# Kernel tuning notes

Measured on AMD Instinct MI355X. Metric: run time of the kernel, lower is better.

## Reference

```python
import jax, jax.numpy as jnp
import numpy as np

B, T, D_IN, D_OUT, D_CTX, A_HID, L_CTX = 32, 256, 512, 512, 512, 512, 128


def setup_inputs() -> dict:
    key = jax.random.key(0)
    ks = jax.random.split(key, 10)
    s = 0.05  # small init scale to avoid gate saturation
    return {
        "x": jax.random.normal(ks[0], (B, T, D_IN), jnp.float32),
        "context": jax.random.normal(ks[1], (B, L_CTX, D_CTX), jnp.float32),
        "W": jax.random.normal(ks[2], (D_IN, 4 * D_OUT), jnp.float32) * s,
        "V": jax.random.normal(ks[3], (D_CTX, 4 * D_OUT), jnp.float32) * s,
        "U": jax.random.normal(ks[4], (D_OUT, 4 * D_OUT), jnp.float32) * s,
        "b": jnp.concatenate([
            jnp.zeros((D_OUT,), jnp.float32),        # b_i
            jnp.ones((D_OUT,), jnp.float32),         # b_f (forget bias init = ones)
            jnp.zeros((2 * D_OUT,), jnp.float32),    # b_c, b_o
        ]),
        "W_h_att": jax.random.normal(ks[5], (D_OUT, A_HID), jnp.float32) * s,
        "W_ctx_att": jax.random.normal(ks[6], (D_CTX, A_HID), jnp.float32) * s,
        "b_att": jnp.zeros((A_HID,), jnp.float32),
        "w_att_prj": jax.random.normal(ks[7], (A_HID, 1), jnp.float32) * s,
    }


def reference(x, context, W, V, U, b, W_h_att, W_ctx_att, b_att, w_att_prj):
    D = U.shape[0]  # output_dim
    # Precompute attention-projected context: (B, L, A)
    att_ctx = jnp.einsum("blc,ca->bla", context, W_ctx_att) + b_att
    # Precompute input contribution for all timesteps: (B, T, 4D)
    xW = jnp.einsum("btd,dk->btk", x, W)

    h0 = jnp.zeros((x.shape[0], D), x.dtype)
    c0 = jnp.zeros((x.shape[0], D), x.dtype)

    def step(carry, xw_t):
        h, c = carry
        # soft attention over context
        h_att = h @ W_h_att                                  # (B, A)
        preprj = jnp.tanh(h_att[:, None, :] + att_ctx)        # (B, L, A)
        prj = jnp.squeeze(preprj @ w_att_prj, -1)             # (B, L)
        alpha = jax.nn.softmax(prj, axis=-1)
        wctx = jnp.einsum("bl,blc->bc", alpha, context)       # (B, C)
        # LSTM gates; slice order follows the original step():
        # i=0, f=1, o=slice 2, candidate=slice 3
        preact = xw_t + wctx @ V + h @ U + b                  # (B, 4D)
        i = jax.nn.sigmoid(preact[:, :D])
        f = jax.nn.sigmoid(preact[:, D:2 * D])
        o = jax.nn.sigmoid(preact[:, 2 * D:3 * D])
        cand = jnp.tanh(preact[:, 3 * D:])
        c_new = f * c + i * cand
        h_new = o * jnp.tanh(c_new)
        return (h_new, c_new), h_new

    xw_seq = jnp.swapaxes(xW, 0, 1)                           # (T, B, 4D)
    _, hs = jax.lax.scan(step, (h0, c0), xw_seq)
    return jnp.swapaxes(hs, 0, 1)                             # (B, T, D)
```

## Files before the change

### kernel.cpp

```cpp
#include <hip/hip_runtime.h>
#include <hip/hip_fp16.h>

#define GD 256
#define BD 1024

constexpr int TSTEPS = 256;
constexpr int DD = 512;
constexpr int LC = 128;

constexpr size_t OFF_FLAGS_F = 0;
constexpr size_t OFF_REL_F   = 8192;
constexpr size_t OFF_GFLG_F  = 8448;
constexpr size_t OFF_HUX     = 16640;
constexpr size_t OFF_SCP     = 82176;
constexpr size_t OFF_H16_F   = 213248;
constexpr size_t HO_HX    = 0;
constexpr size_t HO_ATT   = 16384;
constexpr size_t HO_U16   = 2113536;
constexpr size_t HO_WH16  = 3162112;
constexpr size_t HO_CTXV  = 3424256;
constexpr size_t HO_XW    = 11812864;

typedef _Float16 h16;
typedef _Float16 h2  __attribute__((ext_vector_type(2)));
typedef _Float16 h8v __attribute__((ext_vector_type(8)));
union H8  { h8v v; h2 p[4]; };
union H2U { h2 h; unsigned u; };
union HSU { h16 h; unsigned short u; };

__device__ __forceinline__ float rcp_fast(float x) { return __builtin_amdgcn_rcpf(x); }
__device__ __forceinline__ float ftanh(float x) {
  float e = __expf(2.0f * x);
  return 1.0f - 2.0f * rcp_fast(e + 1.0f);
}
__device__ __forceinline__ float fsig(float x) { return rcp_fast(1.0f + __expf(-x)); }
__device__ __forceinline__ float fdot2(h2 a, h2 b, float c) {
  return __builtin_amdgcn_fdot2(a, b, c, false);
}

__device__ __forceinline__ float cloadf(const float* p) {
  return __hip_atomic_load(p, __ATOMIC_RELAXED, __HIP_MEMORY_SCOPE_AGENT);
}
__device__ __forceinline__ unsigned cloadu(const unsigned* p) {
  return __hip_atomic_load(p, __ATOMIC_RELAXED, __HIP_MEMORY_SCOPE_AGENT);
}
__device__ __forceinline__ void cstoref(float* p, float v) {
  __hip_atomic_store(p, v, __ATOMIC_RELAXED, __HIP_MEMORY_SCOPE_AGENT);
}
__device__ __forceinline__ void cstoreu(unsigned* p, unsigned v) {
  __hip_atomic_store(p, v, __ATOMIC_RELAXED, __HIP_MEMORY_SCOPE_AGENT);
}
__device__ __forceinline__ void cstoreu8(unsigned long long* p, unsigned long long v) {
  __hip_atomic_store(p, v, __ATOMIC_RELAXED, __HIP_MEMORY_SCOPE_AGENT);
}
__device__ __forceinline__ void cstores(h16* p, h16 v) {
  HSU s; s.h = v;
  __hip_atomic_store((unsigned short*)p, s.u, __ATOMIC_RELAXED,
                     __HIP_MEMORY_SCOPE_AGENT);
}

__device__ __forceinline__ void gsync(int* flags, int* rel, int w, int& gen) {
  __syncthreads();
  gen++;
  const int t = threadIdx.x;
  if (w == 0) {
    if (t < 64) {
      if (t == 0)
        __hip_atomic_store(flags, gen, __ATOMIC_RELAXED, __HIP_MEMORY_SCOPE_AGENT);
      for (;;) {
        int m = gen;
#pragma unroll
        for (int i = 0; i < 4; i++) {
          int v = __hip_atomic_load(flags + (t + i * 64) * 32,
                                    __ATOMIC_RELAXED, __HIP_MEMORY_SCOPE_AGENT);
          m = (v < m) ? v : m;
        }
        if (__all(m >= gen)) break;
      }
      if (t == 0) {
#pragma unroll
        for (int i = 0; i < 8; i++)
          __hip_atomic_store(rel + i * 32, gen, __ATOMIC_RELAXED,
                             __HIP_MEMORY_SCOPE_AGENT);
      }
    }
    asm volatile("" ::: "memory");
  } else {
    if (t == 0) {
      __hip_atomic_store(flags + w * 32, gen, __ATOMIC_RELAXED,
                         __HIP_MEMORY_SCOPE_AGENT);
      const int* r = rel + (w & 7) * 32;
      while (__hip_atomic_load(r, __ATOMIC_RELAXED, __HIP_MEMORY_SCOPE_AGENT) < gen)
        __builtin_amdgcn_s_sleep(1);
    }
    asm volatile("" ::: "memory");
  }
  __syncthreads();
}

__device__ __forceinline__ void gbar32(int* gf, int j, int& sg) {
  __syncthreads();
  sg++;
  const int t = threadIdx.x;
  if (t < 64) {
    if (t == 0)
      __hip_atomic_store(gf + j * 32, sg, __ATOMIC_RELAXED,
                         __HIP_MEMORY_SCOPE_AGENT);
    for (;;) {
      int v = sg;
      if (t < 32)
        v = __hip_atomic_load(gf + t * 32, __ATOMIC_RELAXED,
                              __HIP_MEMORY_SCOPE_AGENT);
      if (__all(v >= sg)) break;
      __builtin_amdgcn_s_sleep(1);
    }
  }
  asm volatile("" ::: "memory");
  __syncthreads();
}

__global__ __launch_bounds__(BD, 4) void attn_lstm_persistent(
    const float* __restrict__ x, const float* __restrict__ ctx,
    const float* __restrict__ W, const float* __restrict__ V,
    const float* __restrict__ U, const float* __restrict__ bias,
    const float* __restrict__ Wh, const float* __restrict__ Wc,
    const float* __restrict__ batt, const float* __restrict__ wprj,
    float* __restrict__ out, float* __restrict__ ws) {
  __shared__ __align__(16) unsigned char smem[58448];
  h16*   attcL = (h16*)smem;
  float* red   = (float*)(smem + 18432);
  float* red2  = (float*)(smem + 34816);
  h2*    hLDS  = (h2*)(smem + 51200);
  float* sl    = (float*)(smem + 55296);
  h2*    anL   = (h2*)(smem + 55808);
  float* hattL = (float*)(smem + 56064);
  float* wpL   = (float*)(smem + 56320);
  float* biasS = (float*)(smem + 56384);
  float* pre   = (float*)(smem + 57408);
  float* zinvS = (float*)(smem + 58432);

  const int w = blockIdx.x;
  const int t = threadIdx.x;
  const int xg = w & 7;
  const int j  = w >> 3;
  const int q2 = j >> 3;
  const int bb = 4 * xg + q2;
  const int oct = j & 7;

  int* flags = (int*)(ws + OFF_FLAGS_F);
  int* rel   = (int*)(ws + OFF_REL_F);
  int* gfl   = (int*)(ws + OFF_GFLG_F) + xg * 1024;
  float* hUX = ws + OFF_HUX;
  float* scP = ws + OFF_SCP;
  h16* hb16  = (h16*)(ws + OFF_H16_F);
  h16* hX    = hb16 + HO_HX;
  h16* att16 = hb16 + HO_ATT;
  h16* ctxVp = hb16 + HO_CTXV;
  h16* xw16  = hb16 + HO_XW;

  int gen = 0, sg = 0;
  float c_reg = 0.f;

  {
    const int kp = w;
    {
      const float* r0p = U + (size_t)(2 * kp) * 2048;
      const float* r1p = r0p + 2048;
      const int col0 = 2 * t;
      float u00 = r0p[col0], u01 = r0p[col0 + 1];
      float u10 = r1p[col0], u11 = r1p[col0 + 1];
      int oc  = (col0 & 511) >> 6;
      int cc0 = ((col0 >> 9) << 6) | (col0 & 63);
      H2U p0; p0.h = h2{(h16)u00, (h16)u10};
      H2U p1; p1.h = h2{(h16)u01, (h16)u11};
      unsigned long long pk =
          (unsigned long long)p0.u | ((unsigned long long)p1.u << 32);
      cstoreu8((unsigned long long*)((h2*)(hb16 + HO_U16) +
                                     (size_t)oc * 65536 + (size_t)kp * 256 + cc0),
               pk);
    }
    if (t < 512) {
      float w0 = Wh[(size_t)(2 * kp) * DD + t];
      float w1 = Wh[(size_t)(2 * kp + 1) * DD + t];
      H2U pu; pu.h = h2{(h16)w0, (h16)w1};
      cstoreu((unsigned*)((h2*)(hb16 + HO_WH16) + (size_t)(t >> 6) * 16384 +
                          (size_t)kp * 64 + (t & 63)),
              pu.u);
    }
  }
  {
    float* fbuf = (float*)smem;
    const int r0 = w * 16;
#pragma unroll
    for (int i = 0; i < 2; i++) {
      int idx4 = i * BD + t;
      int row = idx4 >> 7, c4 = idx4 & 127;
      ((float4*)fbuf)[idx4] = ((const float4*)(ctx + (size_t)(r0 + row) * DD))[c4];
    }
    __syncthreads();
    const int a0 = t & 511, rh = t >> 9;
    float acc[8];
#pragma unroll
    for (int r = 0; r < 8; r++) acc[r] = 0.f;
    for (int cc = 0; cc < DD; cc++) {
      float wv = Wc[(size_t)cc * DD + a0];
#pragma unroll
      for (int r = 0; r < 8; r++)
        acc[r] += fbuf[(8 * rh + r) * DD + cc] * wv;
    }
    const float ba = batt[a0];
    for (int r = 0; r < 8; r++)
      cstores(att16 + (size_t)(r0 + 8 * rh + r) * DD + a0, (h16)(acc[r] + ba));
    __syncthreads();
  }
  {
    const int bS = w >> 3, octS = w & 7;
    h2* xstage = (h2*)smem;
    for (int chk = 0; chk < 8; chk++) {
      const int st0 = chk * 32;
      {
        const int row = t >> 5, seg = t & 31;
        const float* src = x + ((size_t)bS * TSTEPS + st0 + row) * DD + seg * 16;
        h2* dst = xstage + row * 256 + seg * 8;
#pragma unroll
        for (int q = 0; q < 4; q++) {
          float4 v = *(const float4*)(src + 4 * q);
          dst[2 * q]     = h2{(h16)v.x, (h16)v.y};
          dst[2 * q + 1] = h2{(h16)v.z, (h16)v.w};
        }
      }
      __syncthreads();
      const int cc = t & 255, sq = t >> 8;
      const int col = ((cc >> 6) << 9) + 64 * octS + (cc & 63);
      float acc[8];
#pragma unroll
      for (int jj = 0; jj < 8; jj++) acc[jj] = 0.f;
#pragma unroll 2
      for (int kp = 0; kp < 256; kp++) {
        float w0 = W[(size_t)(2 * kp) * 2048 + col];
        float w1 = W[(size_t)(2 * kp + 1) * 2048 + col];
        h2 wp = h2{(h16)w0, (h16)w1};
#pragma unroll
        for (int jj = 0; jj < 8; jj++)
          acc[jj] = fdot2(xstage[(sq * 8 + jj) * 256 + kp], wp, acc[jj]);
      }
#pragma unroll
      for (int jj = 0; jj < 8; jj++)
        cstores(xw16 + (((size_t)(bS * 8 + octS) * 256) + st0 + sq * 8 + jj) * 256 + cc,
                (h16)acc[jj]);
      __syncthreads();
    }
    for (int chk = 0; chk < 4; chk++) {
      const int l0 = chk * 32;
      {
        const int row = t >> 5, seg = t & 31;
        const float* src = ctx + ((size_t)bS * LC + l0 + row) * DD + seg * 16;
        h2* dst = xstage + row * 256 + seg * 8;
#pragma unroll
        for (int q = 0; q < 4; q++) {
          float4 v = *(const float4*)(src + 4 * q);
          dst[2 * q]     = h2{(h16)v.x, (h16)v.y};
          dst[2 * q + 1] = h2{(h16)v.z, (h16)v.w};
        }
      }
      __syncthreads();
      const int cc = t & 255, lq = t >> 8;
      const int col = ((cc >> 6) << 9) + 64 * octS + (cc & 63);
      float acc[8];
#pragma unroll
      for (int jj = 0; jj < 8; jj++) acc[jj] = 0.f;
#pragma unroll 2
      for (int kp = 0; kp < 256; kp++) {
        float v0 = V[(size_t)(2 * kp) * 2048 + col];
        float v1 = V[(size_t)(2 * kp + 1) * 2048 + col];
        h2 vp = h2{(h16)v0, (h16)v1};
#pragma unroll
        for (int jj = 0; jj < 8; jj++)
          acc[jj] = fdot2(xstage[(lq * 8 + jj) * 256 + kp], vp, acc[jj]);
      }
#pragma unroll
      for (int jj = 0; jj < 8; jj++)
        cstores(ctxVp + (((size_t)(bS * 8 + octS) * 128) + l0 + lq * 8 + jj) * 256 + cc,
                (h16)acc[jj]);
      __syncthreads();
    }
  }
  gsync(flags, rel, w, gen);

  const int ccL = t & 63, kseg = t >> 6;
  const int aL = t & 15, ks2 = t >> 4;
  h2 u[16], wh[4], cvp01[8], cvp23[8];
  {
    const h2* Ub = (const h2*)(hb16 + HO_U16) + (size_t)(j & 7) * 65536 +
                   (size_t)(j >> 3) * 64 + ccL;
#pragma unroll
    for (int i = 0; i < 16; i++) u[i] = Ub[(size_t)(16 * kseg + i) * 256];
    const h2* Wb = (const h2*)(hb16 + HO_WH16) + (size_t)(j >> 2) * 16384 +
                   16 * (j & 3) + aL;
#pragma unroll
    for (int i = 0; i < 4; i++) wh[i] = Wb[(size_t)(4 * ks2 + i) * 64];
  }
  {
    const int ccg = t & 31, lq = t >> 5;
    const h16* cvb = ctxVp + ((size_t)(bb * 8 + oct) * 128) * 256 + ccg * 8;
    H8 p0, p1, p2, p3;
    p0.v = *(const h8v*)(cvb + (size_t)(4 * lq + 0) * 256);
    p1.v = *(const h8v*)(cvb + (size_t)(4 * lq + 1) * 256);
    p2.v = *(const h8v*)(cvb + (size_t)(4 * lq + 2) * 256);
    p3.v = *(const h8v*)(cvb + (size_t)(4 * lq + 3) * 256);
#pragma unroll
    for (int j8 = 0; j8 < 8; j8++) {
      cvp01[j8] = h2{p0.v[j8], p1.v[j8]};
      cvp23[j8] = h2{p2.v[j8], p3.v[j8]};
    }
  }
  {
    const int row = t >> 1, half = t & 1, q = row >> 7, l = row & 127;
    uint4 v = *(const uint4*)(att16 + (size_t)((4 * xg + q) * LC + l) * DD +
                              16 * j + 8 * half);
    unsigned* dp = (unsigned*)(attcL + row * 18 + 8 * half);
    dp[0] = v.x; dp[1] = v.y; dp[2] = v.z; dp[3] = v.w;
  }
  if (t < 16) wpL[t] = wprj[16 * j + t];
  if (t < 256) biasS[t] = bias[(size_t)(t >> 6) * 512 + 64 * oct + (t & 63)];
  __syncthreads();

  for (int step = 0; step < TSTEPS; step++) {
    {
      unsigned hv = 0;
      if (step > 0)
        hv = cloadu((const unsigned*)(hX + (size_t)(4 * xg + (t >> 8)) * DD +
                                      2 * (t & 255)));
      ((unsigned*)hLDS)[t] = hv;
      __syncthreads();
      {
        float f0 = 0.f, f1 = 0.f, f2 = 0.f, f3 = 0.f;
        const int base = 16 * kseg;
#pragma unroll
        for (int i = 0; i < 16; i++) {
          h2 uu = u[i];
          f0 = fdot2(hLDS[base + i], uu, f0);
          f1 = fdot2(hLDS[256 + base + i], uu, f1);
          f2 = fdot2(hLDS[512 + base + i], uu, f2);
          f3 = fdot2(hLDS[768 + base + i], uu, f3);
        }
        red[kseg * 256 + ccL]       = f0;
        red[kseg * 256 + 64 + ccL]  = f1;
        red[kseg * 256 + 128 + ccL] = f2;
        red[kseg * 256 + 192 + ccL] = f3;
      }
      {
        float g0 = 0.f, g1 = 0.f, g2 = 0.f, g3 = 0.f;
        const int base = 4 * ks2;
#pragma unroll
        for (int i = 0; i < 4; i++) {
          h2 ww = wh[i];
          g0 = fdot2(hLDS[base + i], ww, g0);
          g1 = fdot2(hLDS[256 + base + i], ww, g1);
          g2 = fdot2(hLDS[512 + base + i], ww, g2);
          g3 = fdot2(hLDS[768 + base + i], ww, g3);
        }
        red2[ks2 * 64 + aL]      = g0;
        red2[ks2 * 64 + 16 + aL] = g1;
        red2[ks2 * 64 + 32 + aL] = g2;
        red2[ks2 * 64 + 48 + aL] = g3;
      }
      __syncthreads();
      if (t < 256) {
        float s = 0.f;
#pragma unroll
        for (int k = 0; k < 16; k++) s += red[k * 256 + t];
        cstoref(hUX + (size_t)(4 * xg + (t >> 6)) * 2048 + 64 * j + (t & 63), s);
      } else if (t < 320) {
        const int r = t - 256;
        float s = 0.f;
#pragma unroll
        for (int k = 0; k < 64; k++) s += red2[k * 64 + r];
        hattL[r] = s;
      }
      __syncthreads();
      {
        const int row = t >> 1, half = t & 1, q = row >> 7;
        const h16* arow = attcL + row * 18 + 8 * half;
        const float* hb_ = hattL + q * 16 + 8 * half;
        const float* wp_ = wpL + 8 * half;
        float p = 0.f;
#pragma unroll
        for (int aa = 0; aa < 8; aa++)
          p += ftanh((float)arow[aa] + hb_[aa]) * wp_[aa];
        p += __shfl_xor(p, 1);
        if (half == 0)
          cstoref(scP + (size_t)(4 * xg + q) * 4096 + j * 128 + (row & 127), p);
      }
    }
    gbar32(gfl, j, sg);

    {
      float hUv = 0.f, xwv = 0.f;
      if (t < 256) {
        hUv = cloadf(hUX + (size_t)bb * 2048 + (size_t)(t >> 6) * 512 +
                     64 * oct + (t & 63));
        xwv = (float)xw16[(((size_t)(bb * 8 + oct)) * 256 + step) * 256 + t];
      }
#pragma unroll
      for (int r = 0; r < 4; r++)
        red[r * 1024 + t] = cloadf(scP + (size_t)bb * 4096 + r * 1024 + t);
      __syncthreads();
      if (t < 128) {
        float s = 0.f;
#pragma unroll
        for (int jj = 0; jj < 32; jj++) s += red[jj * 128 + t];
        sl[t] = __expf(s);
      }
      __syncthreads();
      if (t < 64) {
        float z = sl[t] + sl[t + 64];
        z += __shfl_xor(z, 32); z += __shfl_xor(z, 16); z += __shfl_xor(z, 8);
        z += __shfl_xor(z, 4);  z += __shfl_xor(z, 2);  z += __shfl_xor(z, 1);
        if (t == 0) *zinvS = rcp_fast(z);
      }
      __syncthreads();
      if (t < 64) {
        float zi = *zinvS;
        anL[t] = h2{(h16)(sl[2 * t] * zi), (h16)(sl[2 * t + 1] * zi)};
      }
      __syncthreads();
      {
        const int ccg = t & 31, lq = t >> 5, w16 = t >> 6;
        h2 a01 = anL[2 * lq], a23 = anL[2 * lq + 1];
        float acc8[8];
#pragma unroll
        for (int j8 = 0; j8 < 8; j8++)
          acc8[j8] = fdot2(a23, cvp23[j8], fdot2(a01, cvp01[j8], 0.f));
#pragma unroll
        for (int j8 = 0; j8 < 8; j8++) acc8[j8] += __shfl_xor(acc8[j8], 32);
        if ((t & 63) < 32) {
#pragma unroll
          for (int j8 = 0; j8 < 8; j8++)
            red[w16 * 256 + ccg * 8 + j8] = acc8[j8];
        }
      }
      __syncthreads();
      if (t < 256) {
        float pvs = 0.f;
#pragma unroll
        for (int k = 0; k < 16; k++) pvs += red[k * 256 + t];
        pre[t] = pvs + hUv + xwv + biasS[t];
      }
      __syncthreads();
      if (t < 64) {
        const int d = t;
        float pi = pre[d], pf = pre[64 + d], po = pre[128 + d], pg = pre[192 + d];
        float ig = fsig(pi), fg = fsig(pf), og = fsig(po), gg = ftanh(pg);
        float cn = fg * c_reg + ig * gg;
        c_reg = cn;
        float hn = og * ftanh(cn);
        out[((size_t)bb * TSTEPS + step) * DD + 64 * oct + d] = hn;
        cstores(hX + (size_t)bb * DD + 64 * oct + d, (h16)hn);
      }
    }
    gbar32(gfl, j, sg);
  }
}

extern "C" void kernel_launch(void* const* d_in, const int* in_sizes, int n_in,
                              void* d_out, int out_size, void* d_ws, size_t ws_size,
                              hipStream_t stream) {
  (void)in_sizes; (void)n_in; (void)out_size; (void)ws_size;
  const float* x    = (const float*)d_in[0];
  const float* ctx  = (const float*)d_in[1];
  const float* W    = (const float*)d_in[2];
  const float* V    = (const float*)d_in[3];
  const float* U    = (const float*)d_in[4];
  const float* b    = (const float*)d_in[5];
  const float* Wh   = (const float*)d_in[6];
  const float* Wc   = (const float*)d_in[7];
  const float* batt = (const float*)d_in[8];
  const float* wprj = (const float*)d_in[9];

  hipMemsetAsync(d_ws, 0, (8192 + 256 + 8192) * sizeof(int), stream);

  hipLaunchKernelGGL(attn_lstm_persistent, dim3(GD), dim3(BD), 0, stream,
                     x, ctx, W, V, U, b, Wh, Wc, batt, wprj,
                     (float*)d_out, (float*)d_ws);
}
```

Baseline: 2.422 ms.

## Repartition recurrent work per batch row to shrink barrier groups to eight blocks

Each block now owns one batch row and one output octant, and computes the full h@U slice for its own gates locally instead of exchanging hU partials through global memory. The per-step group barrier therefore spans only the 8 blocks of a batch row instead of 32, and the hUX global round-trip is removed. In exchange each thread holds 64 U registers and recomputes h@W_h_att with weights read from global memory every step. It also delays the output store by one step and merges softmax phases to cut __syncthreads.

Result: slower. 3.949 ms (+63.1%).

```diff
diff --git a/kernel.cpp b/kernel.cpp
--- a/kernel.cpp
+++ b/kernel.cpp
@@ -11,9 +11,8 @@
 constexpr size_t OFF_FLAGS_F = 0;
 constexpr size_t OFF_REL_F   = 8192;
 constexpr size_t OFF_GFLG_F  = 8448;
-constexpr size_t OFF_HUX     = 16640;
-constexpr size_t OFF_SCP     = 82176;
-constexpr size_t OFF_H16_F   = 213248;
+constexpr size_t OFF_SCP     = 16640;
+constexpr size_t OFF_H16_F   = 49408;
 constexpr size_t HO_HX    = 0;
 constexpr size_t HO_ATT   = 16384;
 constexpr size_t HO_U16   = 2113536;
@@ -98,17 +97,17 @@
   __syncthreads();
 }
 
-__device__ __forceinline__ void gbar32(int* gf, int j, int& sg) {
+__device__ __forceinline__ void gbar8(int* gf, int oct, int& sg) {
   __syncthreads();
   sg++;
   const int t = threadIdx.x;
   if (t < 64) {
     if (t == 0)
-      __hip_atomic_store(gf + j * 32, sg, __ATOMIC_RELAXED,
+      __hip_atomic_store(gf + oct * 32, sg, __ATOMIC_RELAXED,
                          __HIP_MEMORY_SCOPE_AGENT);
     for (;;) {
       int v = sg;
-      if (t < 32)
+      if (t < 8)
         v = __hip_atomic_load(gf + t * 32, __ATOMIC_RELAXED,
                               __HIP_MEMORY_SCOPE_AGENT);
       if (__all(v >= sg)) break;
@@ -126,31 +125,28 @@
     const float* __restrict__ Wh, const float* __restrict__ Wc,
     const float* __restrict__ batt, const float* __restrict__ wprj,
     float* __restrict__ out, float* __restrict__ ws) {
-  __shared__ __align__(16) unsigned char smem[58448];
+  __shared__ __align__(16) unsigned char smem[46848];
   h16*   attcL = (h16*)smem;
-  float* red   = (float*)(smem + 18432);
-  float* red2  = (float*)(smem + 34816);
-  h2*    hLDS  = (h2*)(smem + 51200);
-  float* sl    = (float*)(smem + 55296);
-  h2*    anL   = (h2*)(smem + 55808);
-  float* hattL = (float*)(smem + 56064);
-  float* wpL   = (float*)(smem + 56320);
-  float* biasS = (float*)(smem + 56384);
-  float* pre   = (float*)(smem + 57408);
-  float* zinvS = (float*)(smem + 58432);
+  float* red   = (float*)(smem + 16896);
+  float* red2  = (float*)(smem + 33280);
+  h2*    hLDS  = (h2*)(smem + 37376);
+  float* hUk   = (float*)(smem + 38400);
+  float* spp   = (float*)(smem + 39424);
+  float* sl    = (float*)(smem + 43520);
+  h2*    anL   = (h2*)(smem + 44032);
+  float* hattL = (float*)(smem + 44288);
+  float* wpL   = (float*)(smem + 44544);
+  float* biasS = (float*)(smem + 44800);
+  float* pre   = (float*)(smem + 45824);
 
   const int w = blockIdx.x;
   const int t = threadIdx.x;
-  const int xg = w & 7;
-  const int j  = w >> 3;
-  const int q2 = j >> 3;
-  const int bb = 4 * xg + q2;
-  const int oct = j & 7;
+  const int b = w >> 3;
+  const int oct = w & 7;
 
   int* flags = (int*)(ws + OFF_FLAGS_F);
   int* rel   = (int*)(ws + OFF_REL_F);
-  int* gfl   = (int*)(ws + OFF_GFLG_F) + xg * 1024;
-  float* hUX = ws + OFF_HUX;
+  int* gfl   = (int*)(ws + OFF_GFLG_F) + b * 256;
   float* scP = ws + OFF_SCP;
   h16* hb16  = (h16*)(ws + OFF_H16_F);
   h16* hX    = hb16 + HO_HX;
@@ -160,6 +156,7 @@
 
   int gen = 0, sg = 0;
   float c_reg = 0.f;
+  float hn_prev = 0.f;
 
   {
     const int kp = w;
@@ -287,22 +284,16 @@
   }
   gsync(flags, rel, w, gen);
 
-  const int ccL = t & 63, kseg = t >> 6;
-  const int aL = t & 15, ks2 = t >> 4;
-  h2 u[16], wh[4], cvp01[8], cvp23[8];
-  {
-    const h2* Ub = (const h2*)(hb16 + HO_U16) + (size_t)(j & 7) * 65536 +
-                   (size_t)(j >> 3) * 64 + ccL;
-#pragma unroll
-    for (int i = 0; i < 16; i++) u[i] = Ub[(size_t)(16 * kseg + i) * 256];
-    const h2* Wb = (const h2*)(hb16 + HO_WH16) + (size_t)(j >> 2) * 16384 +
-                   16 * (j & 3) + aL;
-#pragma unroll
-    for (int i = 0; i < 4; i++) wh[i] = Wb[(size_t)(4 * ks2 + i) * 64];
+  const int ccT = t & 255, kq = t >> 8;
+  h2 u[64], cvp01[8], cvp23[8];
+  {
+    const h2* Ub = (const h2*)(hb16 + HO_U16) + (size_t)oct * 65536 + ccT;
+#pragma unroll
+    for (int i = 0; i < 64; i++) u[i] = Ub[(size_t)(64 * kq + i) * 256];
   }
   {
     const int ccg = t & 31, lq = t >> 5;
-    const h16* cvb = ctxVp + ((size_t)(bb * 8 + oct) * 128) * 256 + ccg * 8;
+    const h16* cvb = ctxVp + ((size_t)(b * 8 + oct) * 128) * 256 + ccg * 8;
     H8 p0, p1, p2, p3;
     p0.v = *(const h8v*)(cvb + (size_t)(4 * lq + 0) * 256);
     p1.v = *(const h8v*)(cvb + (size_t)(4 * lq + 1) * 256);
@@ -315,113 +306,90 @@
     }
   }
   {
-    const int row = t >> 1, half = t & 1, q = row >> 7, l = row & 127;
-    uint4 v = *(const uint4*)(att16 + (size_t)((4 * xg + q) * LC + l) * DD +
-                              16 * j + 8 * half);
-    unsigned* dp = (unsigned*)(attcL + row * 18 + 8 * half);
+    const int l = t >> 3, as = t & 7;
+    uint4 v = *(const uint4*)(att16 + (size_t)(b * LC + l) * DD + 64 * oct + 8 * as);
+    unsigned* dp = (unsigned*)(attcL + l * 66 + 8 * as);
     dp[0] = v.x; dp[1] = v.y; dp[2] = v.z; dp[3] = v.w;
   }
-  if (t < 16) wpL[t] = wprj[16 * j + t];
+  if (t < 64) wpL[t] = wprj[64 * oct + t];
   if (t < 256) biasS[t] = bias[(size_t)(t >> 6) * 512 + 64 * oct + (t & 63)];
   __syncthreads();
 
+  const h2* WhB = (const h2*)(hb16 + HO_WH16) + (size_t)oct * 16384;
+
   for (int step = 0; step < TSTEPS; step++) {
+    float xwv = 0.f;
+
+    if (t < 64 && step > 0)
+      out[((size_t)b * TSTEPS + step - 1) * DD + 64 * oct + t] = hn_prev;
+
     {
-      unsigned hv = 0;
-      if (step > 0)
-        hv = cloadu((const unsigned*)(hX + (size_t)(4 * xg + (t >> 8)) * DD +
-                                      2 * (t & 255)));
-      ((unsigned*)hLDS)[t] = hv;
-      __syncthreads();
-      {
-        float f0 = 0.f, f1 = 0.f, f2 = 0.f, f3 = 0.f;
-        const int base = 16 * kseg;
-#pragma unroll
-        for (int i = 0; i < 16; i++) {
-          h2 uu = u[i];
-          f0 = fdot2(hLDS[base + i], uu, f0);
-          f1 = fdot2(hLDS[256 + base + i], uu, f1);
-          f2 = fdot2(hLDS[512 + base + i], uu, f2);
-          f3 = fdot2(hLDS[768 + base + i], uu, f3);
+      if (t < 256) {
+        unsigned hv = 0;
+        if (step > 0) hv = cloadu((const unsigned*)(hX + (size_t)b * DD + 2 * t));
+        ((unsigned*)hLDS)[t] = hv;
+      }
+      __syncthreads();
+      {
+        float f0 = 0.f, f1 = 0.f;
+        const int base = 64 * kq;
+#pragma unroll
+        for (int i = 0; i < 32; i++) f0 = fdot2(hLDS[base + i], u[i], f0);
+#pragma unroll
+        for (int i = 32; i < 64; i++) f1 = fdot2(hLDS[base + i], u[i], f1);
+        red[kq * 256 + ccT] = f0 + f1;
+      }
+      {
+        const int aL = t & 63, ks = t >> 6;
+        float g0 = 0.f;
+#pragma unroll
+        for (int i = 0; i < 16; i++)
+          g0 = fdot2(hLDS[16 * ks + i], WhB[(size_t)(16 * ks + i) * 64 + aL], g0);
+        red2[ks * 64 + aL] = g0;
+      }
+      if (t < 256)
+        xwv = (float)xw16[(((size_t)(b * 8 + oct)) * 256 + step) * 256 + t];
+      __syncthreads();
+      if (t < 256) {
+        hUk[t] = red[t] + red[256 + t] + red[512 + t] + red[768 + t];
+      } else if (t < 320) {
+        const int a = t - 256;
+        float s = 0.f;
+#pragma unroll
+        for (int k = 0; k < 16; k++) s += red2[k * 64 + a];
+        hattL[a] = s;
+      }
+      __syncthreads();
+      {
+        const int l = t >> 3, as = t & 7;
+        const h16* arow = attcL + l * 66 + 8 * as;
+        float p = 0.f;
+#pragma unroll
+        for (int aa = 0; aa < 8; aa++)
+          p += ftanh((float)arow[aa] + hattL[8 * as + aa]) * wpL[8 * as + aa];
+        p += __shfl_xor(p, 1); p += __shfl_xor(p, 2); p += __shfl_xor(p, 4);
+        if (as == 0)
+          cstoref(scP + (size_t)b * 1024 + oct * 128 + l, p);
+      }
+    }
+    gbar8(gfl, oct, sg);
+
+    {
+      spp[t] = cloadf(scP + (size_t)b * 1024 + t);
+      __syncthreads();
+      if (t < 64) {
+        float s0 = 0.f, s1 = 0.f;
+#pragma unroll
+        for (int o = 0; o < 8; o++) {
+          s0 += spp[o * 128 + t];
+          s1 += spp[o * 128 + 64 + t];
         }
-        red[kseg * 256 + ccL]       = f0;
-        red[kseg * 256 + 64 + ccL]  = f1;
-        red[kseg * 256 + 128 + ccL] = f2;
-        red[kseg * 256 + 192 + ccL] = f3;
-      }
-      {
-        float g0 = 0.f, g1 = 0.f, g2 = 0.f, g3 = 0.f;
-        const int base = 4 * ks2;
-#pragma unroll
-        for (int i = 0; i < 4; i++) {
-          h2 ww = wh[i];
-          g0 = fdot2(hLDS[base + i], ww, g0);
-          g1 = fdot2(hLDS[256 + base + i], ww, g1);
-          g2 = fdot2(hLDS[512 + base + i], ww, g2);
-          g3 = fdot2(hLDS[768 + base + i], ww, g3);
-        }
-        red2[ks2 * 64 + aL]      = g0;
-        red2[ks2 * 64 + 16 + aL] = g1;
-        red2[ks2 * 64 + 32 + aL] = g2;
-        red2[ks2 * 64 + 48 + aL] = g3;
-      }
-      __syncthreads();
-      if (t < 256) {
-        float s = 0.f;
-#pragma unroll
-        for (int k = 0; k < 16; k++) s += red[k * 256 + t];
-        cstoref(hUX + (size_t)(4 * xg + (t >> 6)) * 2048 + 64 * j + (t & 63), s);
-      } else if (t < 320) {
-        const int r = t - 256;
-        float s = 0.f;
-#pragma unroll
-        for (int k = 0; k < 64; k++) s += red2[k * 64 + r];
-        hattL[r] = s;
-      }
-      __syncthreads();
-      {
-        const int row = t >> 1, half = t & 1, q = row >> 7;
-        const h16* arow = attcL + row * 18 + 8 * half;
-        const float* hb_ = hattL + q * 16 + 8 * half;
-        const float* wp_ = wpL + 8 * half;
-        float p = 0.f;
-#pragma unroll
-        for (int aa = 0; aa < 8; aa++)
-          p += ftanh((float)arow[aa] + hb_[aa]) * wp_[aa];
-        p += __shfl_xor(p, 1);
-        if (half == 0)
-          cstoref(scP + (size_t)(4 * xg + q) * 4096 + j * 128 + (row & 127), p);
-      }
-    }
-    gbar32(gfl, j, sg);
-
-    {
-      float hUv = 0.f, xwv = 0.f;
-      if (t < 256) {
-        hUv = cloadf(hUX + (size_t)bb * 2048 + (size_t)(t >> 6) * 512 +
-                     64 * oct + (t & 63));
-        xwv = (float)xw16[(((size_t)(bb * 8 + oct)) * 256 + step) * 256 + t];
-      }
-#pragma unroll
-      for (int r = 0; r < 4; r++)
-        red[r * 1024 + t] = cloadf(scP + (size_t)bb * 4096 + r * 1024 + t);
-      __syncthreads();
-      if (t < 128) {
-        float s = 0.f;
-#pragma unroll
-        for (int jj = 0; jj < 32; jj++) s += red[jj * 128 + t];
-        sl[t] = __expf(s);
-      }
-      __syncthreads();
-      if (t < 64) {
-        float z = sl[t] + sl[t + 64];
+        float e0 = __expf(s0), e1 = __expf(s1);
+        sl[t] = e0; sl[64 + t] = e1;
+        float z = e0 + e1;
         z += __shfl_xor(z, 32); z += __shfl_xor(z, 16); z += __shfl_xor(z, 8);
         z += __shfl_xor(z, 4);  z += __shfl_xor(z, 2);  z += __shfl_xor(z, 1);
-        if (t == 0) *zinvS = rcp_fast(z);
-      }
-      __syncthreads();
-      if (t < 64) {
-        float zi = *zinvS;
+        float zi = rcp_fast(z);
         anL[t] = h2{(h16)(sl[2 * t] * zi), (h16)(sl[2 * t + 1] * zi)};
       }
       __syncthreads();
@@ -445,7 +413,7 @@
         float pvs = 0.f;
 #pragma unroll
         for (int k = 0; k < 16; k++) pvs += red[k * 256 + t];
-        pre[t] = pvs + hUv + xwv + biasS[t];
+        pre[t] = pvs + hUk[t] + xwv + biasS[t];
       }
       __syncthreads();
       if (t < 64) {
@@ -455,12 +423,14 @@
         float cn = fg * c_reg + ig * gg;
         c_reg = cn;
         float hn = og * ftanh(cn);
-        out[((size_t)bb * TSTEPS + step) * DD + 64 * oct + d] = hn;
-        cstores(hX + (size_t)bb * DD + 64 * oct + d, (h16)hn);
-      }
-    }
-    gbar32(gfl, j, sg);
-  }
+        hn_prev = hn;
+        cstores(hX + (size_t)b * DD + 64 * oct + d, (h16)hn);
+      }
+    }
+    gbar8(gfl, oct, sg);
+  }
+  if (t < 64)
+    out[((size_t)b * TSTEPS + TSTEPS - 1) * DD + 64 * oct + t] = hn_prev;
 }
 
 extern "C" void kernel_launch(void* const* d_in, const int* in_sizes, int n_in,
```
